# Performance work log

Measured on AMD Instinct MI355X. Metric: run time of the kernel, lower is better.

Reference implementation:

```python
import jax, jax.numpy as jnp
import numpy as np

N, D, K = 65536, 256, 4096
INIT_COUNT = 100  # torch: counts = ones(K, int32) * 100


def setup_inputs() -> dict:
    key = jax.random.key(0)
    k1, k2 = jax.random.split(key)
    embedded = jax.random.normal(k1, (N, D), dtype=jnp.float32)
    centers = jax.random.normal(k2, (K, D), dtype=jnp.float32)
    counts = jnp.full((K,), INIT_COUNT, dtype=jnp.int32)
    return {"embedded": embedded, "centers": centers, "counts": counts}


def reference(embedded, centers, counts):
    # --- predict_hard: squared euclidean distance [N,K] + argmin ---
    x2 = jnp.sum(embedded * embedded, axis=1, keepdims=True)       # [N,1]
    c2 = jnp.sum(centers * centers, axis=1)                        # [K]
    d2 = x2 - 2.0 * (embedded @ centers.T) + c2                    # [N,K]
    labels = jnp.argmin(d2, axis=1).astype(jnp.int32)              # [N]

    # --- dcn_loss: mean over batch of squared dist to assigned center ---
    loss = jnp.sum((embedded - centers[labels]) ** 2) / embedded.shape[0]

    # --- update_centroids: sequential running-mean update, closed form ---
    # c <- (1-1/n)c + (1/n)x repeated over assigned samples collapses to
    # (count0 * c0 + sum_assigned x) / (count0 + m)
    seg_sum = jax.ops.segment_sum(embedded, labels, num_segments=K)            # [K,D]
    seg_cnt = jax.ops.segment_sum(
        jnp.ones((embedded.shape[0],), dtype=embedded.dtype), labels, num_segments=K
    )                                                                           # [K]
    c0 = counts.astype(embedded.dtype)                                          # [K]
    new_centers = (c0[:, None] * centers + seg_sum) / (c0 + seg_cnt)[:, None]  # [K,D]
    new_counts = counts + seg_cnt.astype(jnp.int32)                             # [K]
    return labels, new_centers, new_counts, loss
```

## Files before the change

kernel.cpp:

```cpp
#include <hip/hip_runtime.h>
#include <cfloat>
#include <cstdint>

constexpr int N  = 65536;
constexpr int D  = 256;
constexpr int K  = 4096;

typedef __attribute__((ext_vector_type(8))) _Float16 half8;
typedef __attribute__((ext_vector_type(8))) unsigned short ushort8;
typedef __attribute__((ext_vector_type(4))) float floatx4;

__device__ __forceinline__ floatx4 mfma_f16(half8 a, half8 b, floatx4 c) {
    return __builtin_amdgcn_mfma_f32_16x16x32_f16(a, b, c, 0, 0, 0);
}

__device__ __forceinline__ void ld_lds16(void* lds, const void* g) {
    __builtin_amdgcn_global_load_lds(
        (const __attribute__((address_space(1))) unsigned int*)g,
        (__attribute__((address_space(3))) unsigned int*)lds, 16, 0, 0);
}

__global__ void prep_c2(const float* __restrict__ C, float* __restrict__ c2) {
    int k = blockIdx.x;
    int l = threadIdx.x;
    const float4* row = (const float4*)(C + (size_t)k * D);
    float4 v = row[l];
    float s = v.x*v.x + v.y*v.y + v.z*v.z + v.w*v.w;
    #pragma unroll
    for (int m = 1; m < 64; m <<= 1) s += __shfl_xor(s, m);
    if (l == 0) c2[k] = s;
}

__global__ void convert_f16_both(const float* __restrict__ X, const float* __restrict__ C,
                                 unsigned short* __restrict__ Xh,
                                 unsigned short* __restrict__ Ch,
                                 float* __restrict__ xsq_part) {
    __shared__ float red[4];
    int id = blockIdx.x * 256 + threadIdx.x;
    const int nX = N * D / 8;
    bool isX = id < nX;
    const float* src; unsigned short* dst;
    if (isX) { src = X; dst = Xh; }
    else     { src = C; dst = Ch; id -= nX; }
    const float4* s4 = (const float4*)src;
    float4 a = s4[2*id], b = s4[2*id+1];
    float xs[8] = {a.x,a.y,a.z,a.w,b.x,b.y,b.z,b.w};
    ushort8 h;
    float ps = 0.f;
    #pragma unroll
    for (int i = 0; i < 8; ++i) {
        union { _Float16 f; unsigned short u; } cv;
        cv.f = (_Float16)xs[i];
        h[i] = cv.u;
        ps += xs[i]*xs[i];
    }
    ((ushort8*)dst)[id] = h;
    if (isX) {
        #pragma unroll
        for (int m = 1; m < 64; m <<= 1) ps += __shfl_xor(ps, m);
        int t = threadIdx.x;
        if ((t & 63) == 0) red[t >> 6] = ps;
        __syncthreads();
        if (t == 0) xsq_part[blockIdx.x] = (red[0] + red[1]) + (red[2] + red[3]);
    }
}

__global__ __launch_bounds__(256, 2) void mfma_assign(
        const unsigned short* __restrict__ Xh, const unsigned short* __restrict__ Ch,
        const float* __restrict__ c2, float* __restrict__ cand)
{
    __shared__ __align__(16) unsigned short sA[8*128*4*8];
    __shared__ __align__(16) unsigned short sB[2*128*4*8];

    const int t    = threadIdx.x;
    const int w    = t >> 6, l = t & 63;
    const int quad = l >> 4, lr = l & 15;
    const int wm   = w >> 1, wn = w & 1;
    const int rowbase = blockIdx.x * 128;
    const int kb   = blockIdx.y;

    const int rl  = l >> 2;
    const int gsw = (l & 3) ^ ((l >> 3) & 3);

    #pragma unroll
    for (int k = 0; k < 2; ++k) {
        int q = 2*w + k;
        const unsigned short* gp = Ch + (size_t)(kb*1024 + q*16 + rl)*D + gsw*8;
        ld_lds16((char*)sB + q*1024, gp);
    }
    #pragma unroll
    for (int k = 0; k < 16; ++k) {
        int q = w*16 + k;
        int c = q >> 3, rb = (q & 7) * 16;
        const unsigned short* gp = Xh + (size_t)(rowbase + rb + rl)*D + c*32 + gsw*8;
        ld_lds16((char*)sA + q*1024, gp);
    }

    const int sA_off = ((64*wm + lr)*4 + (quad ^ ((lr>>1)&3)))*16;
    const int sB_off = ((64*wn + lr)*4 + (quad ^ ((lr>>1)&3)))*16;

    float v1[16], v2[16]; int x1[16], x2s[16];
    #pragma unroll
    for (int i = 0; i < 16; ++i) { v1[i]=FLT_MAX; v2[i]=FLT_MAX; x1[i]=0x7fffffff; x2s[i]=0x7fffffff; }

    floatx4 acc[4][4];
    float c2v[4]; int jidx[4];
    int buf = 0;

    for (int chunk = 0; chunk < 64; ++chunk) {
        const int dk = chunk & 7;
        const int ct = kb*8 + (chunk >> 3);

        if (dk == 0) {
            #pragma unroll
            for (int i = 0; i < 4; ++i)
                #pragma unroll
                for (int j = 0; j < 4; ++j) acc[i][j] = (floatx4)0.f;
            const int colbase = ct*128 + 64*wn;
            #pragma unroll
            for (int j = 0; j < 4; ++j) {
                int col = colbase + 16*j + lr;
                c2v[j] = c2[col]; jidx[j] = col;
            }
        }

        __syncthreads();

        if (chunk < 63) {
            int nc = chunk + 1;
            int nct = kb*8 + (nc >> 3), ndk = nc & 7;
            #pragma unroll
            for (int k = 0; k < 2; ++k) {
                int q = 2*w + k;
                const unsigned short* gp = Ch + (size_t)(nct*128 + q*16 + rl)*D + ndk*32 + gsw*8;
                ld_lds16((char*)sB + (buf^1)*8192 + q*1024, gp);
            }
        }

        half8 Af[4], Bf[4];
        #pragma unroll
        for (int i = 0; i < 4; ++i)
            Af[i] = *(const half8*)((const char*)sA + dk*8192 + i*1024 + sA_off);
        #pragma unroll
        for (int j = 0; j < 4; ++j)
            Bf[j] = *(const half8*)((const char*)sB + buf*8192 + j*1024 + sB_off);
        #pragma unroll
        for (int j = 0; j < 4; ++j)
            #pragma unroll
            for (int i = 0; i < 4; ++i)
                acc[i][j] = mfma_f16(Af[i], Bf[j], acc[i][j]);

        if (dk == 7) {
            #pragma unroll
            for (int i = 0; i < 4; ++i)
                #pragma unroll
                for (int j = 0; j < 4; ++j)
                    #pragma unroll
                    for (int r = 0; r < 4; ++r) {
                        float s = fmaf(-2.f, acc[i][j][r], c2v[j]);
                        int st = 4*i + r;
                        bool cA = s < v1[st];
                        bool cB = s < v2[st];
                        float tv = cB ? s : v2[st]; int tx = cB ? jidx[j] : x2s[st];
                        v2[st] = cA ? v1[st] : tv;  x2s[st] = cA ? x1[st] : tx;
                        v1[st] = cA ? s : v1[st];   x1[st]  = cA ? jidx[j] : x1[st];
                    }
        }
        buf ^= 1;
    }

    #pragma unroll
    for (int i = 0; i < 4; ++i)
        #pragma unroll
        for (int r = 0; r < 4; ++r) {
            int st = 4*i + r;
            float a1 = v1[st], a2 = v2[st]; int ax1 = x1[st], ax2 = x2s[st];
            #pragma unroll
            for (int m = 1; m < 16; m <<= 1) {
                float b1f = __shfl_xor(a1, m); int bx1 = __shfl_xor(ax1, m);
                float b2f = __shfl_xor(a2, m); int bx2 = __shfl_xor(ax2, m);
                bool tt = (b1f < a1) || (b1f == a1 && bx1 < ax1);
                float n1 = tt ? b1f : a1; int nx1 = tt ? bx1 : ax1;
                float w1 = tt ? a1 : b1f; int wx1 = tt ? ax1 : bx1;
                float w2 = tt ? b2f : a2; int wx2 = tt ? bx2 : ax2;
                bool uu = (w2 < w1) || (w2 == w1 && wx2 < wx1);
                a1 = n1; ax1 = nx1;
                a2 = uu ? w2 : w1; ax2 = uu ? wx2 : wx1;
            }
            if (lr == 0) {
                int row = rowbase + 64*wm + 16*i + 4*quad + r;
                float4 o; o.x = a1; o.y = __int_as_float(ax1);
                o.z = a2; o.w = __int_as_float(ax2);
                ((float4*)cand)[(size_t)row*8 + 2*kb + wn] = o;
            }
        }
}

__global__ __launch_bounds__(256) void recheck_label(
        const float* __restrict__ X, const float* __restrict__ C,
        const float* __restrict__ c2, const float* __restrict__ cand,
        float* __restrict__ out_labels, int* __restrict__ labInt,
        int* __restrict__ cnt)
{
    int t = threadIdx.x, w = t >> 6, l = t & 63;
    int row = blockIdx.x * 4 + w;

    float s = FLT_MAX; int idx = 0x7fffffff;
    if (l < 16) {
        float4 e = ((const float4*)cand)[(size_t)row*8 + (l >> 1)];
        s   = (l & 1) ? e.z : e.x;
        idx = (l & 1) ? __float_as_int(e.w) : __float_as_int(e.y);
    }

    float a1 = s, a2 = FLT_MAX; int ax1 = idx, ax2 = 0x7fffffff;
    #pragma unroll
    for (int m = 1; m < 16; m <<= 1) {
        float b1 = __shfl_xor(a1, m); int bx1 = __shfl_xor(ax1, m);
        float b2 = __shfl_xor(a2, m); int bx2 = __shfl_xor(ax2, m);
        bool tt = (b1 < a1) || (b1 == a1 && bx1 < ax1);
        float n1 = tt ? b1 : a1; int nx1 = tt ? bx1 : ax1;
        float w1 = tt ? a1 : b1; int wx1 = tt ? ax1 : bx1;
        float w2 = tt ? b2 : a2; int wx2 = tt ? bx2 : ax2;
        bool uu = (w2 < w1) || (w2 == w1 && wx2 < wx1);
        a1 = n1; ax1 = nx1;
        a2 = uu ? w2 : w1; ax2 = uu ? wx2 : wx1;
    }
    float s1 = __shfl(a1, 0), s2 = __shfl(a2, 0);
    int   i1 = __shfl(ax1, 0);

    int label;
    if (s2 - s1 > 0.25f) {
        label = i1;
    } else {
        float4 xv = ((const float4*)X)[(size_t)row*64 + l];
        float px = xv.x*xv.x + xv.y*xv.y + xv.z*xv.z + xv.w*xv.w;
        #pragma unroll
        for (int m = 1; m < 64; m <<= 1) px += __shfl_xor(px, m);
        bool active = (l < 16) && (s <= s1 + 0.25f);
        unsigned long long mask = __ballot(active);
        float best = FLT_MAX; int bi = 0x7fffffff;
        while (mask) {
            int k = __ffsll((long long)mask) - 1;
            mask &= mask - 1;
            int ck = __shfl(idx, k);
            float4 cv = ((const float4*)C)[(size_t)ck*64 + l];
            float pd = xv.x*cv.x + xv.y*cv.y + xv.z*cv.z + xv.w*cv.w;
            #pragma unroll
            for (int m = 1; m < 64; m <<= 1) pd += __shfl_xor(pd, m);
            float d2 = fmaf(-2.f, pd, px) + c2[ck];
            if (d2 < best || (d2 == best && ck < bi)) { best = d2; bi = ck; }
        }
        label = bi;
    }

    if (l == 0) {
        out_labels[row] = (float)label;
        labInt[row] = label;
        atomicAdd(&cnt[label], 1);
    }
}

__global__ void prefix_kernel(const int* __restrict__ cnt,
                              int* __restrict__ offs, int* __restrict__ cursor) {
    int l = threadIdx.x;
    int s = 0;
    #pragma unroll 8
    for (int i = 0; i < 64; ++i) s += cnt[l*64 + i];
    int inc = s;
    #pragma unroll
    for (int off = 1; off < 64; off <<= 1) {
        int u = __shfl_up(inc, off);
        if (l >= off) inc += u;
    }
    int run = inc - s;
    for (int i = 0; i < 64; ++i) {
        int k = l*64 + i;
        offs[k] = run; cursor[k] = run;
        run += cnt[k];
    }
}

__global__ void scatter_idx(const int* __restrict__ labInt,
                            int* __restrict__ cursor, int* __restrict__ sortedIdx) {
    int i = blockIdx.x * 256 + threadIdx.x;
    int lab = labInt[i];
    int pos = atomicAdd(&cursor[lab], 1);
    sortedIdx[pos] = i;
}

__global__ __launch_bounds__(256) void center_update(
        const float* __restrict__ X, const float* __restrict__ C,
        const int* __restrict__ counts0, const int* __restrict__ cnt,
        const int* __restrict__ offs, const int* __restrict__ sortedIdx,
        float* __restrict__ lossC, float* __restrict__ out)
{
    __shared__ float red[4];
    int k = blockIdx.x, d = threadIdx.x;
    int start = offs[k], m = cnt[k];
    float acc = 0.f;
    int i = 0;
    for (; i + 4 <= m; i += 4) {
        int r0 = sortedIdx[start+i],   r1 = sortedIdx[start+i+1];
        int r2 = sortedIdx[start+i+2], r3 = sortedIdx[start+i+3];
        float a0 = X[(size_t)r0*D + d], a1 = X[(size_t)r1*D + d];
        float a2 = X[(size_t)r2*D + d], a3 = X[(size_t)r3*D + d];
        acc += (a0 + a1) + (a2 + a3);
    }
    for (; i < m; ++i) acc += X[(size_t)sortedIdx[start+i]*D + d];

    float cv = C[(size_t)k*D + d];
    float c0 = (float)counts0[k];
    out[N + (size_t)k*D + d] = (c0 * cv + acc) / (c0 + (float)m);
    if (d == 0) out[N + (size_t)K*D + k] = (float)(counts0[k] + m);

    float lp = cv * fmaf((float)m, cv, -2.f*acc);
    #pragma unroll
    for (int s = 1; s < 64; s <<= 1) lp += __shfl_xor(lp, s);
    if ((d & 63) == 0) red[d >> 6] = lp;
    __syncthreads();
    if (d == 0) lossC[k] = (red[0] + red[1]) + (red[2] + red[3]);
}

__global__ __launch_bounds__(256) void loss_final(
        const float* __restrict__ xsq_part, const float* __restrict__ lossC,
        float* __restrict__ out)
{
    __shared__ double red[4];
    int t = threadIdx.x;
    double s = 0.0;
    for (int i = t; i < 8192; i += 256) s += (double)xsq_part[i];
    for (int i = t; i < 4096; i += 256) s += (double)lossC[i];
    #pragma unroll
    for (int m = 1; m < 64; m <<= 1) s += __shfl_xor(s, m);
    if ((t & 63) == 0) red[t >> 6] = s;
    __syncthreads();
    if (t == 0)
        out[N + (size_t)K*D + K] = (float)(((red[0] + red[1]) + (red[2] + red[3])) / (double)N);
}

__global__ void finalize_kernel(const float* __restrict__ C,
                                const int* __restrict__ counts0,
                                const float* __restrict__ seg,
                                const int* __restrict__ cnt,
                                const double* __restrict__ lossAcc,
                                float* __restrict__ out)
{
    int g = blockIdx.x * 256 + threadIdx.x;
    int k = g >> 8;
    float c0 = (float)counts0[k];
    float m  = (float)cnt[k];
    out[N + g] = (c0 * C[g] + seg[g]) / (c0 + m);
    if (g < K) out[N + (size_t)K*D + g] = (float)(counts0[g] + cnt[g]);
    if (g == 0) out[N + (size_t)K*D + K] = (float)(lossAcc[0] / (double)N);
}

__global__ __launch_bounds__(256, 2) void assign_fp32(
        const float* __restrict__ X, const float* __restrict__ C,
        const float* __restrict__ c2, float* __restrict__ out_labels,
        float* __restrict__ seg, int* __restrict__ cnt,
        double* __restrict__ lossAcc)
{
    constexpr int BM = 128, BN = 128, KD = 16;
    __shared__ float As[KD][BM];
    __shared__ float Bs[KD][BN];
    __shared__ float x2f[BM];
    __shared__ int   labs[BM];

    const int t  = threadIdx.x;
    const int tx = t & 15;
    const int ty = t >> 4;
    const int rowbase = blockIdx.x * BM;

    {
        int r  = t >> 1;
        int dh = (t & 1) * (D / 2);
        const float4* xr = (const float4*)(X + (size_t)(rowbase + r) * D + dh);
        float s = 0.f;
        #pragma unroll
        for (int i = 0; i < D / 8; ++i) {
            float4 v = xr[i];
            s += v.x*v.x + v.y*v.y + v.z*v.z + v.w*v.w;
        }
        s += __shfl_xor(s, 1);
        if ((t & 1) == 0) x2f[r] = s;
    }
    __syncthreads();

    float x2v[8];
    #pragma unroll
    for (int i = 0; i < 4; ++i) { x2v[i] = x2f[4*ty + i]; x2v[i+4] = x2f[64 + 4*ty + i]; }

    float rmv[8]; int rmi[8];
    #pragma unroll
    for (int i = 0; i < 8; ++i) { rmv[i] = FLT_MAX; rmi[i] = 0x7fffffff; }

    for (int ct = 0; ct < K / BN; ++ct) {
        float acc[8][8];
        #pragma unroll
        for (int i = 0; i < 8; ++i)
            #pragma unroll
            for (int j = 0; j < 8; ++j) acc[i][j] = 0.f;

        float c2f2[8];
        {
            float4 a = *(const float4*)(c2 + ct*BN + 4*tx);
            float4 b = *(const float4*)(c2 + ct*BN + 64 + 4*tx);
            c2f2[0]=a.x; c2f2[1]=a.y; c2f2[2]=a.z; c2f2[3]=a.w;
            c2f2[4]=b.x; c2f2[5]=b.y; c2f2[6]=b.z; c2f2[7]=b.w;
        }

        for (int dk = 0; dk < D / KD; ++dk) {
            #pragma unroll
            for (int i = 0; i < 2; ++i) {
                int f  = t + 256 * i;
                int r  = f >> 2;
                int dp = f & 3;
                float4 av = *(const float4*)(X + (size_t)(rowbase + r) * D + dk*KD + 4*dp);
                float4 bv = *(const float4*)(C + (size_t)(ct*BN + r) * D + dk*KD + 4*dp);
                As[4*dp+0][r]=av.x; As[4*dp+1][r]=av.y; As[4*dp+2][r]=av.z; As[4*dp+3][r]=av.w;
                Bs[4*dp+0][r]=bv.x; Bs[4*dp+1][r]=bv.y; Bs[4*dp+2][r]=bv.z; Bs[4*dp+3][r]=bv.w;
            }
            __syncthreads();
            #pragma unroll
            for (int kk = 0; kk < KD; ++kk) {
                float4 a0 = *(const float4*)&As[kk][4*ty];
                float4 a1 = *(const float4*)&As[kk][64 + 4*ty];
                float4 b0 = *(const float4*)&Bs[kk][4*tx];
                float4 b1 = *(const float4*)&Bs[kk][64 + 4*tx];
                float av[8] = {a0.x,a0.y,a0.z,a0.w,a1.x,a1.y,a1.z,a1.w};
                float bv[8] = {b0.x,b0.y,b0.z,b0.w,b1.x,b1.y,b1.z,b1.w};
                #pragma unroll
                for (int i = 0; i < 8; ++i)
                    #pragma unroll
                    for (int j = 0; j < 8; ++j)
                        acc[i][j] = fmaf(av[i], bv[j], acc[i][j]);
            }
            __syncthreads();
        }

        #pragma unroll
        for (int i = 0; i < 8; ++i) {
            float bv = FLT_MAX; int bi = 0x7fffffff;
            #pragma unroll
            for (int j = 0; j < 8; ++j) {
                int coll = (j < 4) ? (4*tx + j) : (64 + 4*tx + (j - 4));
                float v = fmaf(-2.f, acc[i][j], x2v[i]) + c2f2[j];
                int idx = ct * BN + coll;
                if (v < bv || (v == bv && idx < bi)) { bv = v; bi = idx; }
            }
            #pragma unroll
            for (int m = 1; m < 16; m <<= 1) {
                float ov = __shfl_xor(bv, m);
                int   oi = __shfl_xor(bi, m);
                if (ov < bv || (ov == bv && oi < bi)) { bv = ov; bi = oi; }
            }
            if (bv < rmv[i] || (bv == rmv[i] && bi < rmi[i])) { rmv[i] = bv; rmi[i] = bi; }
        }
    }

    if (tx == 0) {
        #pragma unroll
        for (int i = 0; i < 8; ++i) {
            int r = (i < 4) ? (4*ty + i) : (64 + 4*ty + (i - 4));
            labs[r] = rmi[i];
            out_labels[rowbase + r] = (float)rmi[i];
            atomicAdd(&cnt[rmi[i]], 1);
        }
    }
    __syncthreads();

    {
        int r   = t >> 1;
        int dh  = (t & 1) * (D / 2);
        int lab = labs[r];
        const float4* xr = (const float4*)(X + (size_t)(rowbase + r) * D + dh);
        const float4* cr = (const float4*)(C + (size_t)lab * D + dh);
        float* sp = seg + (size_t)lab * D + dh;
        float ls = 0.f;
        #pragma unroll 8
        for (int i = 0; i < D / 8; ++i) {
            float4 xv = xr[i];
            float4 cv = cr[i];
            atomicAdd(sp + 4*i + 0, xv.x);
            atomicAdd(sp + 4*i + 1, xv.y);
            atomicAdd(sp + 4*i + 2, xv.z);
            atomicAdd(sp + 4*i + 3, xv.w);
            float d0 = xv.x - cv.x, d1 = xv.y - cv.y;
            float d2 = xv.z - cv.z, d3 = xv.w - cv.w;
            ls += d0*d0 + d1*d1 + d2*d2 + d3*d3;
        }
        #pragma unroll
        for (int m = 1; m < 64; m <<= 1) ls += __shfl_xor(ls, m);
        if ((t & 63) == 0) atomicAdd(lossAcc, (double)ls);
    }
}

extern "C" void kernel_launch(void* const* d_in, const int* in_sizes, int n_in,
                              void* d_out, int out_size, void* d_ws, size_t ws_size,
                              hipStream_t stream) {
    const float* X       = (const float*)d_in[0];
    const float* C       = (const float*)d_in[1];
    const int*   counts0 = (const int*)d_in[2];
    float* out = (float*)d_out;

    char* p = (char*)d_ws;
    float*  seg     = (float*)p;          p += (size_t)K * D * 4;
    int*    cnt     = (int*)p;            p += (size_t)K * 4;
    float*  c2      = (float*)p;          p += (size_t)K * 4;
    double* lossAcc = (double*)p;         p += 16;
    size_t zero_all = (size_t)(p - (char*)d_ws);
    float*  cand    = (float*)p;          p += (size_t)N * 32 * 4;
    unsigned short* Xh = (unsigned short*)p; p += (size_t)N * D * 2;
    unsigned short* Ch = (unsigned short*)p; p += (size_t)K * D * 2;
    float* xsq_part = (float*)p;          p += 8192 * 4;
    float* lossC    = (float*)p;          p += (size_t)K * 4;
    size_t need = (size_t)(p - (char*)d_ws);

    int* labInt    = (int*)seg;
    int* sortedIdx = labInt + N;
    int* offs      = sortedIdx + N;
    int* cursor    = offs + K;

    if (ws_size >= need) {
        hipMemsetAsync(cnt, 0, (size_t)K * 4, stream);
        prep_c2<<<K, 64, 0, stream>>>(C, c2);
        convert_f16_both<<<(N*D/8 + K*D/8)/256, 256, 0, stream>>>(X, C, Xh, Ch, xsq_part);
        mfma_assign<<<dim3(N/128, 4), 256, 0, stream>>>(Xh, Ch, c2, cand);
        recheck_label<<<N/4, 256, 0, stream>>>(X, C, c2, cand, out, labInt, cnt);
        prefix_kernel<<<1, 64, 0, stream>>>(cnt, offs, cursor);
        scatter_idx<<<N/256, 256, 0, stream>>>(labInt, cursor, sortedIdx);
        center_update<<<K, 256, 0, stream>>>(X, C, counts0, cnt, offs, sortedIdx, lossC, out);
        loss_final<<<1, 256, 0, stream>>>(xsq_part, lossC, out);
    } else {
        hipMemsetAsync(d_ws, 0, zero_all, stream);
        prep_c2<<<K, 64, 0, stream>>>(C, c2);
        assign_fp32<<<N/128, 256, 0, stream>>>(X, C, c2, out, seg, cnt, lossAcc);
        finalize_kernel<<<(K*D)/256, 256, 0, stream>>>(C, counts0, seg, cnt, lossAcc, out);
    }
}
```

Baseline: 574.3 us.

## Fuse c2 into f16 conversion, pack four rows per wave in recheck

```diff
diff --git a/kernel.cpp b/kernel.cpp
--- a/kernel.cpp
+++ b/kernel.cpp
@@ -34,7 +34,8 @@
 __global__ void convert_f16_both(const float* __restrict__ X, const float* __restrict__ C,
                                  unsigned short* __restrict__ Xh,
                                  unsigned short* __restrict__ Ch,
-                                 float* __restrict__ xsq_part) {
+                                 float* __restrict__ xsq_part,
+                                 float* __restrict__ c2) {
     __shared__ float red[4];
     int id = blockIdx.x * 256 + threadIdx.x;
     const int nX = N * D / 8;
@@ -55,13 +56,17 @@
         ps += xs[i]*xs[i];
     }
     ((ushort8*)dst)[id] = h;
+    int t = threadIdx.x;
     if (isX) {
         #pragma unroll
         for (int m = 1; m < 64; m <<= 1) ps += __shfl_xor(ps, m);
-        int t = threadIdx.x;
         if ((t & 63) == 0) red[t >> 6] = ps;
         __syncthreads();
         if (t == 0) xsq_part[blockIdx.x] = (red[0] + red[1]) + (red[2] + red[3]);
+    } else {
+        #pragma unroll
+        for (int m = 1; m < 32; m <<= 1) ps += __shfl_xor(ps, m);
+        if ((t & 31) == 0) c2[id >> 5] = ps;
     }
 }
 
@@ -96,6 +101,8 @@
         ld_lds16((char*)sA + q*1024, gp);
     }
 
+    const unsigned short* gpB = Ch + (size_t)(kb*1024 + 2*w*16 + rl)*D + gsw*8 + 32;
+
     const int sA_off = ((64*wm + lr)*4 + (quad ^ ((lr>>1)&3)))*16;
     const int sB_off = ((64*wn + lr)*4 + (quad ^ ((lr>>1)&3)))*16;
 
@@ -128,13 +135,9 @@
 
         if (chunk < 63) {
             int nc = chunk + 1;
-            int nct = kb*8 + (nc >> 3), ndk = nc & 7;
-            #pragma unroll
-            for (int k = 0; k < 2; ++k) {
-                int q = 2*w + k;
-                const unsigned short* gp = Ch + (size_t)(nct*128 + q*16 + rl)*D + ndk*32 + gsw*8;
-                ld_lds16((char*)sB + (buf^1)*8192 + q*1024, gp);
-            }
+            ld_lds16((char*)sB + (buf^1)*8192 + (2*w+0)*1024, gpB);
+            ld_lds16((char*)sB + (buf^1)*8192 + (2*w+1)*1024, gpB + 16*D);
+            gpB += ((nc & 7) == 7) ? (size_t)(128*D - 7*32) : 32;
         }
 
         half8 Af[4], Bf[4];
@@ -203,14 +206,14 @@
         int* __restrict__ cnt)
 {
     int t = threadIdx.x, w = t >> 6, l = t & 63;
-    int row = blockIdx.x * 4 + w;
-
-    float s = FLT_MAX; int idx = 0x7fffffff;
-    if (l < 16) {
-        float4 e = ((const float4*)cand)[(size_t)row*8 + (l >> 1)];
-        s   = (l & 1) ? e.z : e.x;
-        idx = (l & 1) ? __float_as_int(e.w) : __float_as_int(e.y);
-    }
+    int g  = l >> 4;
+    int lr = l & 15;
+    int row0 = (blockIdx.x * 4 + w) * 4;
+    int row  = row0 + g;
+
+    float4 e = ((const float4*)cand)[(size_t)row*8 + (lr >> 1)];
+    float s  = (lr & 1) ? e.z : e.x;
+    int  idx = (lr & 1) ? __float_as_int(e.w) : __float_as_int(e.y);
 
     float a1 = s, a2 = FLT_MAX; int ax1 = idx, ax2 = 0x7fffffff;
     #pragma unroll
@@ -225,24 +228,36 @@
         a1 = n1; ax1 = nx1;
         a2 = uu ? w2 : w1; ax2 = uu ? wx2 : wx1;
     }
-    float s1 = __shfl(a1, 0), s2 = __shfl(a2, 0);
-    int   i1 = __shfl(ax1, 0);
-
-    int label;
-    if (s2 - s1 > 0.25f) {
-        label = i1;
-    } else {
-        float4 xv = ((const float4*)X)[(size_t)row*64 + l];
+
+    bool certain = (a2 - a1 > 0.25f);
+    unsigned long long certMask = __ballot(certain);
+
+    if (certain && lr == 0) {
+        out_labels[row] = (float)ax1;
+        labInt[row] = ax1;
+        atomicAdd(&cnt[ax1], 1);
+    }
+
+    #pragma unroll
+    for (int q = 0; q < 4; ++q) {
+        if ((certMask >> (q*16)) & 1ull) continue;
+        int r = row0 + q;
+        float sq  = __shfl(s,   q*16 + lr);
+        int   iq  = __shfl(idx, q*16 + lr);
+        float gs1 = __shfl(a1,  q*16);
+
+        float4 xv = ((const float4*)X)[(size_t)r*64 + l];
         float px = xv.x*xv.x + xv.y*xv.y + xv.z*xv.z + xv.w*xv.w;
         #pragma unroll
         for (int m = 1; m < 64; m <<= 1) px += __shfl_xor(px, m);
-        bool active = (l < 16) && (s <= s1 + 0.25f);
+
+        bool active = (l < 16) && (sq <= gs1 + 0.25f);
         unsigned long long mask = __ballot(active);
         float best = FLT_MAX; int bi = 0x7fffffff;
         while (mask) {
             int k = __ffsll((long long)mask) - 1;
             mask &= mask - 1;
-            int ck = __shfl(idx, k);
+            int ck = __shfl(iq, k);
             float4 cv = ((const float4*)C)[(size_t)ck*64 + l];
             float pd = xv.x*cv.x + xv.y*cv.y + xv.z*cv.z + xv.w*cv.w;
             #pragma unroll
@@ -250,13 +265,11 @@
             float d2 = fmaf(-2.f, pd, px) + c2[ck];
             if (d2 < best || (d2 == best && ck < bi)) { best = d2; bi = ck; }
         }
-        label = bi;
-    }
-
-    if (l == 0) {
-        out_labels[row] = (float)label;
-        labInt[row] = label;
-        atomicAdd(&cnt[label], 1);
+        if (l == 0) {
+            out_labels[r] = (float)bi;
+            labInt[r] = bi;
+            atomicAdd(&cnt[bi], 1);
+        }
     }
 }
 
@@ -523,10 +536,9 @@
 
     if (ws_size >= need) {
         hipMemsetAsync(cnt, 0, (size_t)K * 4, stream);
-        prep_c2<<<K, 64, 0, stream>>>(C, c2);
-        convert_f16_both<<<(N*D/8 + K*D/8)/256, 256, 0, stream>>>(X, C, Xh, Ch, xsq_part);
+        convert_f16_both<<<(N*D/8 + K*D/8)/256, 256, 0, stream>>>(X, C, Xh, Ch, xsq_part, c2);
         mfma_assign<<<dim3(N/128, 4), 256, 0, stream>>>(Xh, Ch, c2, cand);
-        recheck_label<<<N/4, 256, 0, stream>>>(X, C, c2, cand, out, labInt, cnt);
+        recheck_label<<<N/16, 256, 0, stream>>>(X, C, c2, cand, out, labInt, cnt);
         prefix_kernel<<<1, 64, 0, stream>>>(cnt, offs, cursor);
         scatter_idx<<<N/256, 256, 0, stream>>>(labInt, cursor, sortedIdx);
         center_update<<<K, 256, 0, stream>>>(X, C, counts0, cnt, offs, sortedIdx, lossC, out);
```

After: 572.0 us. Within noise of the previous version (-0.4%).
